# Optimization experiments

Measured on AMD Instinct MI355X. Metric: run time of the kernel, lower is better.

The kernel has to match this reference:

```python
import jax, jax.numpy as jnp
import numpy as np

N = 100000   # nodes
E = 3200000  # edges (avg degree 32)
F_IN = 767   # Amazon-Computers num_features
H = 16       # hidden (constructor default x=16)
C = 10       # num_classes


def setup_inputs() -> dict:
    key = jax.random.key(0)
    ks = jax.random.split(key, 12)
    def w(k, shape):
        fan_in = shape[0]
        return jax.random.normal(k, shape, jnp.float32) / np.sqrt(fan_in)
    return {
        "x": jax.random.normal(ks[0], (N, F_IN), jnp.float32),
        "edge_index": jax.random.randint(ks[1], (2, E), 0, N, jnp.int32),
        "w1_init": w(ks[2], (F_IN, H)), "w1_root": w(ks[3], (F_IN, H)), "b1": jnp.zeros((H,), jnp.float32),
        "w2_init": w(ks[4], (H, H)),    "w2_root": w(ks[5], (H, H)),    "b2": jnp.zeros((H,), jnp.float32),
        "w3_init": w(ks[6], (H, C)),    "w3_root": w(ks[7], (H, C)),    "b3": jnp.zeros((C,), jnp.float32),
    }


def _gcn_norm(row, col, dtype):
    # PyG ARMAConv: gcn_norm without self-loops: norm_e = deg^{-1/2}[row] * deg^{-1/2}[col]
    deg = jax.ops.segment_sum(jnp.ones((E,), dtype), col, num_segments=N)
    dinv = jnp.where(deg > 0, deg ** -0.5, 0.0)
    return dinv[row] * dinv[col]


def _arma_conv(x, w_init, w_root, b, row, col, norm):
    # K=1 stack, T=1 layer: relu( A_hat @ (x W_init) + x W_root + b )
    h = x @ w_init                                   # [N, F_out]
    msg = h[row] * norm[:, None]                     # [E, F_out] irregular gather
    agg = jax.ops.segment_sum(msg, col, num_segments=N)  # scatter-add to targets
    return jax.nn.relu(agg + x @ w_root + b)


def reference(x, edge_index, w1_init, w1_root, b1, w2_init, w2_root, b2, w3_init, w3_root, b3):
    row, col = edge_index[0], edge_index[1]
    norm = _gcn_norm(row, col, x.dtype)
    # Net.forward (eval mode: dropout = identity). Outer relu after conv1/conv2 is
    # idempotent with ARMAConv's internal relu but kept for faithfulness.
    h = jax.nn.relu(_arma_conv(x, w1_init, w1_root, b1, row, col, norm))
    h = jax.nn.relu(_arma_conv(h, w2_init, w2_root, b2, row, col, norm))
    h = _arma_conv(h, w3_init, w3_root, b3, row, col, norm)
    return jax.nn.log_softmax(h, axis=1)
```

## Files before the change

kernel.cpp:

```cpp
#include <hip/hip_runtime.h>
#include <hip/hip_bf16.h>
#include <cstdint>
#include <cstddef>

#define F_IN 767
#define HD   16

typedef __attribute__((ext_vector_type(8))) short short8v;
typedef __attribute__((ext_vector_type(4))) float float4v;
typedef float __attribute__((ext_vector_type(4), aligned(4))) float4a;

static __device__ __forceinline__ unsigned short f2bf(float f) {
  unsigned int u = __float_as_uint(f);
  return (unsigned short)((u + 0x7fffu + ((u >> 16) & 1u)) >> 16);
}
static __device__ __forceinline__ float bf2f(unsigned short b) {
  return __uint_as_float(((unsigned int)b) << 16);
}


__global__ void k_hist(const int* __restrict__ col, int* __restrict__ cnt, int E) {
  int e = blockIdx.x * 256 + threadIdx.x;
  if (e < E) atomicAdd(&cnt[col[e]], 1);
}

__global__ void k_scan1(const int* __restrict__ cnt, int* __restrict__ off,
                        int* __restrict__ bsum, int N) {
  __shared__ int lds[256];
  int t = threadIdx.x;
  int base = blockIdx.x * 1024 + t * 4;
  int4 v = make_int4(0, 0, 0, 0);
  if (base + 3 < N) {
    v = *(const int4*)&cnt[base];
  } else {
    if (base + 0 < N) v.x = cnt[base + 0];
    if (base + 1 < N) v.y = cnt[base + 1];
    if (base + 2 < N) v.z = cnt[base + 2];
    if (base + 3 < N) v.w = cnt[base + 3];
  }
  int s = v.x + v.y + v.z + v.w;
  lds[t] = s;
  __syncthreads();
  for (int d = 1; d < 256; d <<= 1) {
    int add = (t >= d) ? lds[t - d] : 0;
    __syncthreads();
    lds[t] += add;
    __syncthreads();
  }
  int excl = lds[t] - s;
  if (t == 255) bsum[blockIdx.x] = lds[255];
  int run = excl;
  if (base + 0 < N) off[base + 0] = run; run += v.x;
  if (base + 1 < N) off[base + 1] = run; run += v.y;
  if (base + 2 < N) off[base + 2] = run; run += v.z;
  if (base + 3 < N) off[base + 3] = run;
}

__global__ void k_scan2(int* __restrict__ bsum, int nb) {
  __shared__ int lds[256];
  int t = threadIdx.x;
  int s = (t < nb) ? bsum[t] : 0;
  lds[t] = s;
  __syncthreads();
  for (int d = 1; d < 256; d <<= 1) {
    int add = (t >= d) ? lds[t - d] : 0;
    __syncthreads();
    lds[t] += add;
    __syncthreads();
  }
  if (t < nb) bsum[t] = lds[t] - s;
}

__global__ void k_scan3(const int* __restrict__ cnt, int* __restrict__ off,
                        int* __restrict__ cur, float* __restrict__ dinv,
                        const int* __restrict__ bsum, int N) {
  int i = blockIdx.x * 256 + threadIdx.x;
  if (i < N) {
    int o = off[i] + bsum[i >> 10];
    off[i] = o;
    cur[i] = o;
    int c = cnt[i];
    dinv[i] = (c > 0) ? rsqrtf((float)c) : 0.f;
  }
}

#define PSH     9
#define PA_TILE 4096

__global__ void k_binit(const int* __restrict__ off, int* __restrict__ bcur, int N, int E) {
  int b = threadIdx.x;
  int cb = b << PSH;
  bcur[b] = (cb < N) ? off[cb] : E;
}

__global__ __launch_bounds__(256) void k_part(const int* __restrict__ row,
                                              const int* __restrict__ col,
                                              int* __restrict__ bcur,
                                              int2* __restrict__ tmp, int E) {
  __shared__ int  hcnt[256];
  __shared__ int  hoff[256];
  __shared__ int  hcur[256];
  __shared__ int  gbase[256];
  __shared__ int2 st[PA_TILE];
  int t = threadIdx.x;
  int tile = blockIdx.x * PA_TILE;
  int nE = min(PA_TILE, E - tile);

  hcnt[t] = 0;
  __syncthreads();

  int r[16], c[16];
  #pragma unroll
  for (int i = 0; i < 16; ++i) {
    int li = i * 256 + t;
    if (li < nE) {
      r[i] = row[tile + li];
      c[i] = col[tile + li];
      atomicAdd(&hcnt[c[i] >> PSH], 1);
    } else c[i] = -1;
  }
  __syncthreads();

  int s = hcnt[t];
  hoff[t] = s;
  __syncthreads();
  for (int d = 1; d < 256; d <<= 1) {
    int add = (t >= d) ? hoff[t - d] : 0;
    __syncthreads();
    hoff[t] += add;
    __syncthreads();
  }
  int excl = hoff[t] - s;
  hcur[t] = excl;
  gbase[t] = (s > 0) ? atomicAdd(&bcur[t], s) : 0;
  __syncthreads();

  #pragma unroll
  for (int i = 0; i < 16; ++i) {
    if (c[i] >= 0) {
      int p = atomicAdd(&hcur[c[i] >> PSH], 1);
      st[p] = make_int2(r[i], c[i]);
    }
  }
  __syncthreads();

  #pragma unroll
  for (int i = 0; i < 16; ++i) {
    int idx = i * 256 + t;
    if (idx < nE) {
      int2 v = st[idx];
      int b = v.y >> PSH;
      tmp[gbase[b] + (idx - (hoff[b] - hcnt[b]))] = v;
    }
  }
}

#define PLS 4
__global__ __launch_bounds__(256) void k_place(const int2* __restrict__ tmp,
                                               const int* __restrict__ off,
                                               int* __restrict__ cur,
                                               int* __restrict__ srow, int N, int E) {
  int b = blockIdx.x / PLS, sp = blockIdx.x % PLS;
  int cb = b << PSH;
  if (cb >= N) return;
  int start = off[cb];
  int nx = (b + 1) << PSH;
  int end = (nx < N) ? off[nx] : E;
  int len = end - start;
  int per = (len + PLS - 1) / PLS;
  int s0 = start + sp * per;
  int s1 = min(s0 + per, end);
  for (int e = s0 + threadIdx.x; e < s1; e += 256) {
    int2 v = tmp[e];
    int p = atomicAdd(&cur[v.y], 1);
    srow[p] = v.x;
  }
}

__global__ void k_pack(const float* __restrict__ wi, const float* __restrict__ wr,
                       float* __restrict__ Wc, int K, int H) {
  int i = blockIdx.x * 256 + threadIdx.x;
  int tot = K * 2 * H;
  if (i < tot) {
    int k = i / (2 * H), c = i % (2 * H);
    Wc[i] = (c < H) ? wi[k * H + c] : wr[k * H + (c - H)];
  }
}

__global__ void k_packbf(const float* __restrict__ wi, const float* __restrict__ wr,
                         unsigned short* __restrict__ Bf) {
  int idx = blockIdx.x * 256 + threadIdx.x;
  if (idx >= 24 * 2 * 2 * 64 * 8) return;
  int j    = idx & 7;
  int l    = (idx >> 3) & 63;
  int half = (idx >> 9) & 1;
  int term = (idx >> 10) & 1;
  int s    = idx >> 11;
  int col  = half * 16 + (l & 15);
  int k    = s * 32 + (l >> 4) * 8 + j;
  float w = 0.f;
  if (k < F_IN) w = (col < 16) ? wi[k * 16 + col] : wr[k * 16 + (col - 16)];
  unsigned short hi = f2bf(w);
  unsigned short lo = f2bf(w - bf2f(hi));
  Bf[idx] = (term == 0) ? hi : lo;
}

__global__ __launch_bounds__(256) void k_gemm1(const float* __restrict__ x,
                                               const unsigned short* __restrict__ Bf,
                                               const float* __restrict__ dinv,
                                               float* __restrict__ T, int N) {
  int t = threadIdx.x;
  int w = t >> 6, l = t & 63;
  int kg = l >> 4;
  int rowA = blockIdx.x * 64 + w * 16 + (l & 15);
  const float* xr = x + (size_t)min(rowA, N - 1) * F_IN;
  const short8v* Bfv = (const short8v*)Bf;

  float4v c0 = {0.f, 0.f, 0.f, 0.f};
  float4v c1 = {0.f, 0.f, 0.f, 0.f};

  for (int s = 0; s < 24; ++s) {
    int kbase = s * 32 + kg * 8;
    float v[8];
    if (s < 23) {
      float4a a = *(const float4a*)(xr + kbase);
      float4a b = *(const float4a*)(xr + kbase + 4);
      v[0] = a.x; v[1] = a.y; v[2] = a.z; v[3] = a.w;
      v[4] = b.x; v[5] = b.y; v[6] = b.z; v[7] = b.w;
    } else {
      #pragma unroll
      for (int j = 0; j < 8; ++j) {
        int k = kbase + j;
        v[j] = (k < F_IN) ? xr[k] : 0.f;
      }
    }
    short8v ah, al;
    #pragma unroll
    for (int j = 0; j < 8; ++j) {
      unsigned short h = f2bf(v[j]);
      ah[j] = (short)h;
      al[j] = (short)f2bf(v[j] - bf2f(h));
    }
    short8v bh0 = Bfv[(s * 4 + 0) * 64 + l];
    short8v bh1 = Bfv[(s * 4 + 1) * 64 + l];
    short8v bl0 = Bfv[(s * 4 + 2) * 64 + l];
    short8v bl1 = Bfv[(s * 4 + 3) * 64 + l];
    c0 = __builtin_amdgcn_mfma_f32_16x16x32_bf16(ah, bh0, c0, 0, 0, 0);
    c1 = __builtin_amdgcn_mfma_f32_16x16x32_bf16(ah, bh1, c1, 0, 0, 0);
    c0 = __builtin_amdgcn_mfma_f32_16x16x32_bf16(al, bh0, c0, 0, 0, 0);
    c1 = __builtin_amdgcn_mfma_f32_16x16x32_bf16(al, bh1, c1, 0, 0, 0);
    c0 = __builtin_amdgcn_mfma_f32_16x16x32_bf16(ah, bl0, c0, 0, 0, 0);
    c1 = __builtin_amdgcn_mfma_f32_16x16x32_bf16(ah, bl1, c1, 0, 0, 0);
  }

  int rowC = blockIdx.x * 64 + w * 16 + (l >> 4) * 4;
  int colC = l & 15;
  #pragma unroll
  for (int j = 0; j < 4; ++j) {
    int gr = rowC + j;
    if (gr < N) {
      float d = dinv[gr];
      T[(size_t)gr * 32 + colC]      = c0[j] * d;
      T[(size_t)gr * 32 + 16 + colC] = c1[j];
    }
  }
}

__global__ void k_gemm_small(const float* __restrict__ h, const float* __restrict__ W,
                             const float* __restrict__ dinv,
                             float* __restrict__ T, int N, int P, int SC) {
  int idx = blockIdx.x * 256 + threadIdx.x;
  int n = idx >> 5, c = idx & 31;
  if (n < N && c < P) {
    float acc = 0.f;
    #pragma unroll
    for (int k = 0; k < HD; ++k) acc += h[(size_t)n * HD + k] * W[k * P + c];
    if (c < SC) acc *= dinv[n];
    T[(size_t)n * P + c] = acc;
  }
}

__global__ void k_gather_relu(const float* __restrict__ T, const int* __restrict__ off,
                              const int* __restrict__ cnt, const int* __restrict__ srow,
                              const float* __restrict__ dinv, const float* __restrict__ bias,
                              float* __restrict__ hout, int N) {
  int t = threadIdx.x;
  int j = t & 15, ln = t >> 4;
  int n = blockIdx.x * 16 + ln;
  if (n >= N) return;
  int s = off[n], c = cnt[n];
  float acc = 0.f;
  int p = s, e4 = s + (c & ~3);
  for (; p < e4; p += 4) {
    int r0 = srow[p], r1 = srow[p + 1], r2 = srow[p + 2], r3 = srow[p + 3];
    float v0 = T[(size_t)r0 * 32 + j];
    float v1 = T[(size_t)r1 * 32 + j];
    float v2 = T[(size_t)r2 * 32 + j];
    float v3 = T[(size_t)r3 * 32 + j];
    acc += v0; acc += v1; acc += v2; acc += v3;
  }
  for (; p < s + c; ++p) acc += T[(size_t)srow[p] * 32 + j];
  float v = dinv[n] * acc + T[(size_t)n * 32 + 16 + j] + bias[j];
  hout[(size_t)n * HD + j] = fmaxf(v, 0.f);
}

__global__ void k_gather_lsm(const float* __restrict__ T, const int* __restrict__ off,
                             const int* __restrict__ cnt, const int* __restrict__ srow,
                             const float* __restrict__ dinv, const float* __restrict__ b3,
                             float* __restrict__ out, int N) {
  int t = threadIdx.x;
  int j = t & 15, ln = t >> 4;
  int n = blockIdx.x * 16 + ln;
  bool act = (n < N) && (j < 10);
  float v = -1e30f;
  if (act) {
    int s = off[n], c = cnt[n];
    float acc = 0.f;
    int p = s, e4 = s + (c & ~3);
    for (; p < e4; p += 4) {
      int r0 = srow[p], r1 = srow[p + 1], r2 = srow[p + 2], r3 = srow[p + 3];
      float v0 = T[(size_t)r0 * 20 + j];
      float v1 = T[(size_t)r1 * 20 + j];
      float v2 = T[(size_t)r2 * 20 + j];
      float v3 = T[(size_t)r3 * 20 + j];
      acc += v0; acc += v1; acc += v2; acc += v3;
    }
    for (; p < s + c; ++p) acc += T[(size_t)srow[p] * 20 + j];
    v = dinv[n] * acc + T[(size_t)n * 20 + 10 + j] + b3[j];
    v = fmaxf(v, 0.f);
  }
  float m = v;
  #pragma unroll
  for (int mask = 8; mask >= 1; mask >>= 1) m = fmaxf(m, __shfl_xor(m, mask, 16));
  float e = act ? __expf(v - m) : 0.f;
  float sum = e;
  #pragma unroll
  for (int mask = 8; mask >= 1; mask >>= 1) sum += __shfl_xor(sum, mask, 16);
  if (act) out[(size_t)n * 10 + j] = (v - m) - __logf(sum);
}

extern "C" void kernel_launch(void* const* d_in, const int* in_sizes, int n_in,
                              void* d_out, int out_size, void* d_ws, size_t ws_size,
                              hipStream_t stream) {
  const float* x    = (const float*)d_in[0];
  const int* eidx   = (const int*)d_in[1];
  const float* w1i  = (const float*)d_in[2];
  const float* w1r  = (const float*)d_in[3];
  const float* b1   = (const float*)d_in[4];
  const float* w2i  = (const float*)d_in[5];
  const float* w2r  = (const float*)d_in[6];
  const float* b2   = (const float*)d_in[7];
  const float* w3i  = (const float*)d_in[8];
  const float* w3r  = (const float*)d_in[9];
  const float* b3   = (const float*)d_in[10];
  float* out = (float*)d_out;

  const int N = in_sizes[0] / F_IN;
  const int E = in_sizes[1] / 2;
  const int* row = eidx;
  const int* col = eidx + E;

  char* p = (char*)d_ws;
  auto alloc = [&](size_t bytes) { void* r = (void*)p; p += (bytes + 255) & ~(size_t)255; return r; };
  int*   cnt  = (int*)alloc((size_t)N * 4);
  int*   off  = (int*)alloc((size_t)N * 4);
  int*   cur  = (int*)alloc((size_t)N * 4);
  float* dinv = (float*)alloc((size_t)N * 4);
  int*   bsum = (int*)alloc(1024);
  int*   bcur = (int*)alloc(1024);
  unsigned short* Bf = (unsigned short*)alloc((size_t)24 * 2 * 2 * 64 * 8 * 2);
  float* W2c  = (float*)alloc((size_t)HD * 32 * 4);
  float* W3c  = (float*)alloc((size_t)HD * 20 * 4);
  int*   srow = (int*)alloc((size_t)E * 4);
  char*  big  = (char*)alloc((size_t)E * 8);
  int2*  tmp  = (int2*)big;
  float* T    = (float*)big;
  float* h    = (float*)(big + (size_t)N * 32 * 4);

  const int nbE = (E + 255) / 256;
  const int nbScan = (N + 1023) / 1024;
  const int nBuck = (N + (1 << PSH) - 1) >> PSH;

  hipMemsetAsync(cnt, 0, (size_t)N * 4, stream);
  k_hist <<<nbE, 256, 0, stream>>>(col, cnt, E);
  k_scan1<<<nbScan, 256, 0, stream>>>(cnt, off, bsum, N);
  k_scan2<<<1, 256, 0, stream>>>(bsum, nbScan);
  k_scan3<<<(N + 255) / 256, 256, 0, stream>>>(cnt, off, cur, dinv, bsum, N);
  k_binit<<<1, 256, 0, stream>>>(off, bcur, N, E);
  k_part <<<(E + PA_TILE - 1) / PA_TILE, 256, 0, stream>>>(row, col, bcur, tmp, E);
  k_place<<<nBuck * PLS, 256, 0, stream>>>(tmp, off, cur, srow, N, E);

  k_packbf<<<192, 256, 0, stream>>>(w1i, w1r, Bf);
  k_pack<<<(HD * 32 + 255) / 256, 256, 0, stream>>>(w2i, w2r, W2c, HD, 16);
  k_pack<<<(HD * 20 + 255) / 256, 256, 0, stream>>>(w3i, w3r, W3c, HD, 10);

  k_gemm1<<<(N + 63) / 64, 256, 0, stream>>>(x, Bf, dinv, T, N);
  k_gather_relu<<<(N + 15) / 16, 256, 0, stream>>>(T, off, cnt, srow, dinv, b1, h, N);
  k_gemm_small<<<(N * 32 + 255) / 256, 256, 0, stream>>>(h, W2c, dinv, T, N, 32, 16);
  k_gather_relu<<<(N + 15) / 16, 256, 0, stream>>>(T, off, cnt, srow, dinv, b2, h, N);
  k_gemm_small<<<(N * 32 + 255) / 256, 256, 0, stream>>>(h, W3c, dinv, T, N, 20, 10);
  k_gather_lsm<<<(N + 15) / 16, 256, 0, stream>>>(T, off, cnt, srow, dinv, b3, out, N);
}
```

Baseline: 934.4 us.

## Fuse small per-layer GEMMs into gather kernels and vectorize histogram

The small dense GEMM for layers 2 and 3 now runs inside the gather kernel, using 16-lane shuffles to form the next layer's transformed features. This removes two launches and the round trip of the intermediate h through global memory. Layer-3 weights are padded to a 32-wide layout so all gathers share one stride, and the gather loops are unrolled to 8. The histogram kernel now reads col as int4, and the place kernel splits each bucket into 8 parts instead of 4.

```diff
diff --git a/kernel.cpp b/kernel.cpp
--- a/kernel.cpp
+++ b/kernel.cpp
@@ -20,8 +20,16 @@
 
 
 __global__ void k_hist(const int* __restrict__ col, int* __restrict__ cnt, int E) {
-  int e = blockIdx.x * 256 + threadIdx.x;
-  if (e < E) atomicAdd(&cnt[col[e]], 1);
+  int base = (blockIdx.x * 256 + threadIdx.x) * 4;
+  if (base + 3 < E) {
+    int4 v = *(const int4*)&col[base];
+    atomicAdd(&cnt[v.x], 1);
+    atomicAdd(&cnt[v.y], 1);
+    atomicAdd(&cnt[v.z], 1);
+    atomicAdd(&cnt[v.w], 1);
+  } else {
+    for (int e = base; e < E; ++e) atomicAdd(&cnt[col[e]], 1);
+  }
 }
 
 __global__ void k_scan1(const int* __restrict__ cnt, int* __restrict__ off,
@@ -155,7 +163,7 @@
   }
 }
 
-#define PLS 4
+#define PLS 8
 __global__ __launch_bounds__(256) void k_place(const int2* __restrict__ tmp,
                                                const int* __restrict__ off,
                                                int* __restrict__ cur,
@@ -177,13 +185,15 @@
   }
 }
 
-__global__ void k_pack(const float* __restrict__ wi, const float* __restrict__ wr,
-                       float* __restrict__ Wc, int K, int H) {
+__global__ void k_pack2(const float* __restrict__ wi, const float* __restrict__ wr,
+                        float* __restrict__ Wc, int P) {
   int i = blockIdx.x * 256 + threadIdx.x;
-  int tot = K * 2 * H;
-  if (i < tot) {
-    int k = i / (2 * H), c = i % (2 * H);
-    Wc[i] = (c < H) ? wi[k * H + c] : wr[k * H + (c - H)];
+  if (i < 16 * 32) {
+    int k = i >> 5, c = i & 31;
+    float v = 0.f;
+    if (c < 16) { if (c < P) v = wi[k * P + c]; }
+    else        { int cc = c - 16; if (cc < P) v = wr[k * P + cc]; }
+    Wc[i] = v;
   }
 }
 
@@ -266,45 +276,44 @@
   }
 }
 
-__global__ void k_gemm_small(const float* __restrict__ h, const float* __restrict__ W,
-                             const float* __restrict__ dinv,
-                             float* __restrict__ T, int N, int P, int SC) {
-  int idx = blockIdx.x * 256 + threadIdx.x;
-  int n = idx >> 5, c = idx & 31;
-  if (n < N && c < P) {
-    float acc = 0.f;
-    #pragma unroll
-    for (int k = 0; k < HD; ++k) acc += h[(size_t)n * HD + k] * W[k * P + c];
-    if (c < SC) acc *= dinv[n];
-    T[(size_t)n * P + c] = acc;
-  }
-}
-
-__global__ void k_gather_relu(const float* __restrict__ T, const int* __restrict__ off,
+__global__ void k_gather_fuse(const float* __restrict__ Tin, const int* __restrict__ off,
                               const int* __restrict__ cnt, const int* __restrict__ srow,
                               const float* __restrict__ dinv, const float* __restrict__ bias,
-                              float* __restrict__ hout, int N) {
+                              const float* __restrict__ W,
+                              float* __restrict__ Tout, int N) {
   int t = threadIdx.x;
   int j = t & 15, ln = t >> 4;
   int n = blockIdx.x * 16 + ln;
   if (n >= N) return;
+  const float* Tj = Tin + j;
   int s = off[n], c = cnt[n];
   float acc = 0.f;
-  int p = s, e4 = s + (c & ~3);
-  for (; p < e4; p += 4) {
-    int r0 = srow[p], r1 = srow[p + 1], r2 = srow[p + 2], r3 = srow[p + 3];
-    float v0 = T[(size_t)r0 * 32 + j];
-    float v1 = T[(size_t)r1 * 32 + j];
-    float v2 = T[(size_t)r2 * 32 + j];
-    float v3 = T[(size_t)r3 * 32 + j];
+  int p = s, e8 = s + (c & ~7);
+  for (; p < e8; p += 8) {
+    int r0 = srow[p],     r1 = srow[p + 1], r2 = srow[p + 2], r3 = srow[p + 3];
+    int r4 = srow[p + 4], r5 = srow[p + 5], r6 = srow[p + 6], r7 = srow[p + 7];
+    float v0 = Tj[(size_t)r0 * 32], v1 = Tj[(size_t)r1 * 32];
+    float v2 = Tj[(size_t)r2 * 32], v3 = Tj[(size_t)r3 * 32];
+    float v4 = Tj[(size_t)r4 * 32], v5 = Tj[(size_t)r5 * 32];
+    float v6 = Tj[(size_t)r6 * 32], v7 = Tj[(size_t)r7 * 32];
     acc += v0; acc += v1; acc += v2; acc += v3;
-  }
-  for (; p < s + c; ++p) acc += T[(size_t)srow[p] * 32 + j];
-  float v = dinv[n] * acc + T[(size_t)n * 32 + 16 + j] + bias[j];
-  hout[(size_t)n * HD + j] = fmaxf(v, 0.f);
-}
-
-__global__ void k_gather_lsm(const float* __restrict__ T, const int* __restrict__ off,
+    acc += v4; acc += v5; acc += v6; acc += v7;
+  }
+  for (; p < s + c; ++p) acc += Tj[(size_t)srow[p] * 32];
+  float d = dinv[n];
+  float h = fmaxf(d * acc + Tin[(size_t)n * 32 + 16 + j] + bias[j], 0.f);
+  float o0 = 0.f, o1 = 0.f;
+  #pragma unroll
+  for (int k = 0; k < 16; ++k) {
+    float hk = __shfl(h, k, 16);
+    o0 += hk * W[k * 32 + j];
+    o1 += hk * W[k * 32 + 16 + j];
+  }
+  Tout[(size_t)n * 32 + j]      = o0 * d;
+  Tout[(size_t)n * 32 + 16 + j] = o1;
+}
+
+__global__ void k_gather_lsm(const float* __restrict__ Tin, const int* __restrict__ off,
                              const int* __restrict__ cnt, const int* __restrict__ srow,
                              const float* __restrict__ dinv, const float* __restrict__ b3,
                              float* __restrict__ out, int N) {
@@ -314,19 +323,22 @@
   bool act = (n < N) && (j < 10);
   float v = -1e30f;
   if (act) {
+    const float* Tj = Tin + j;
     int s = off[n], c = cnt[n];
     float acc = 0.f;
-    int p = s, e4 = s + (c & ~3);
-    for (; p < e4; p += 4) {
-      int r0 = srow[p], r1 = srow[p + 1], r2 = srow[p + 2], r3 = srow[p + 3];
-      float v0 = T[(size_t)r0 * 20 + j];
-      float v1 = T[(size_t)r1 * 20 + j];
-      float v2 = T[(size_t)r2 * 20 + j];
-      float v3 = T[(size_t)r3 * 20 + j];
+    int p = s, e8 = s + (c & ~7);
+    for (; p < e8; p += 8) {
+      int r0 = srow[p],     r1 = srow[p + 1], r2 = srow[p + 2], r3 = srow[p + 3];
+      int r4 = srow[p + 4], r5 = srow[p + 5], r6 = srow[p + 6], r7 = srow[p + 7];
+      float v0 = Tj[(size_t)r0 * 32], v1 = Tj[(size_t)r1 * 32];
+      float v2 = Tj[(size_t)r2 * 32], v3 = Tj[(size_t)r3 * 32];
+      float v4 = Tj[(size_t)r4 * 32], v5 = Tj[(size_t)r5 * 32];
+      float v6 = Tj[(size_t)r6 * 32], v7 = Tj[(size_t)r7 * 32];
       acc += v0; acc += v1; acc += v2; acc += v3;
-    }
-    for (; p < s + c; ++p) acc += T[(size_t)srow[p] * 20 + j];
-    v = dinv[n] * acc + T[(size_t)n * 20 + 10 + j] + b3[j];
+      acc += v4; acc += v5; acc += v6; acc += v7;
+    }
+    for (; p < s + c; ++p) acc += Tj[(size_t)srow[p] * 32];
+    v = dinv[n] * acc + Tin[(size_t)n * 32 + 16 + j] + b3[j];
     v = fmaxf(v, 0.f);
   }
   float m = v;
@@ -369,20 +381,20 @@
   int*   bsum = (int*)alloc(1024);
   int*   bcur = (int*)alloc(1024);
   unsigned short* Bf = (unsigned short*)alloc((size_t)24 * 2 * 2 * 64 * 8 * 2);
-  float* W2c  = (float*)alloc((size_t)HD * 32 * 4);
-  float* W3c  = (float*)alloc((size_t)HD * 20 * 4);
+  float* W2c  = (float*)alloc((size_t)16 * 32 * 4);
+  float* W3c  = (float*)alloc((size_t)16 * 32 * 4);
   int*   srow = (int*)alloc((size_t)E * 4);
   char*  big  = (char*)alloc((size_t)E * 8);
   int2*  tmp  = (int2*)big;
-  float* T    = (float*)big;
-  float* h    = (float*)(big + (size_t)N * 32 * 4);
-
-  const int nbE = (E + 255) / 256;
+  float* T1   = (float*)big;
+  float* T2   = (float*)(big + (size_t)N * 32 * 4);
+  float* T3   = T1;
+
   const int nbScan = (N + 1023) / 1024;
   const int nBuck = (N + (1 << PSH) - 1) >> PSH;
 
   hipMemsetAsync(cnt, 0, (size_t)N * 4, stream);
-  k_hist <<<nbE, 256, 0, stream>>>(col, cnt, E);
+  k_hist <<<(E / 4 + 255) / 256, 256, 0, stream>>>(col, cnt, E);
   k_scan1<<<nbScan, 256, 0, stream>>>(cnt, off, bsum, N);
   k_scan2<<<1, 256, 0, stream>>>(bsum, nbScan);
   k_scan3<<<(N + 255) / 256, 256, 0, stream>>>(cnt, off, cur, dinv, bsum, N);
@@ -391,13 +403,11 @@
   k_place<<<nBuck * PLS, 256, 0, stream>>>(tmp, off, cur, srow, N, E);
 
   k_packbf<<<192, 256, 0, stream>>>(w1i, w1r, Bf);
-  k_pack<<<(HD * 32 + 255) / 256, 256, 0, stream>>>(w2i, w2r, W2c, HD, 16);
-  k_pack<<<(HD * 20 + 255) / 256, 256, 0, stream>>>(w3i, w3r, W3c, HD, 10);
-
-  k_gemm1<<<(N + 63) / 64, 256, 0, stream>>>(x, Bf, dinv, T, N);
-  k_gather_relu<<<(N + 15) / 16, 256, 0, stream>>>(T, off, cnt, srow, dinv, b1, h, N);
-  k_gemm_small<<<(N * 32 + 255) / 256, 256, 0, stream>>>(h, W2c, dinv, T, N, 32, 16);
-  k_gather_relu<<<(N + 15) / 16, 256, 0, stream>>>(T, off, cnt, srow, dinv, b2, h, N);
-  k_gemm_small<<<(N * 32 + 255) / 256, 256, 0, stream>>>(h, W3c, dinv, T, N, 20, 10);
-  k_gather_lsm<<<(N + 15) / 16, 256, 0, stream>>>(T, off, cnt, srow, dinv, b3, out, N);
-}
+  k_pack2<<<2, 256, 0, stream>>>(w2i, w2r, W2c, 16);
+  k_pack2<<<2, 256, 0, stream>>>(w3i, w3r, W3c, 10);
+
+  k_gemm1<<<(N + 63) / 64, 256, 0, stream>>>(x, Bf, dinv, T1, N);
+  k_gather_fuse<<<(N + 15) / 16, 256, 0, stream>>>(T1, off, cnt, srow, dinv, b1, W2c, T2, N);
+  k_gather_fuse<<<(N + 15) / 16, 256, 0, stream>>>(T2, off, cnt, srow, dinv, b2, W3c, T3, N);
+  k_gather_lsm<<<(N + 15) / 16, 256, 0, stream>>>(T3, off, cnt, srow, dinv, b3, out, N);
+}
```

Result: faster. 914.9 us (-2.1%).
